# Kernel tuning notes

Hardware: AMD Instinct MI355X
Metric: run time of the kernel (lower is better)

The kernel has to match this reference:

```python
import jax, jax.numpy as jnp
import numpy as np

B, N, C = 1, 512, 128  # batch, seq (pair rows/cols), pair channel dim
EPS = 1e-5
ENDING = False  # 'outgoing' triangle update (ending=False in the torch module)


def layer_norm(x, w, b):
    mu = jnp.mean(x, axis=-1, keepdims=True)
    var = jnp.mean(jnp.square(x - mu), axis=-1, keepdims=True)
    return (x - mu) * jax.lax.rsqrt(var + EPS) * w + b


def setup_inputs() -> dict:
    key = jax.random.key(0)
    ks = jax.random.split(key, 10)
    s = 0.02
    return {
        "x": jax.random.normal(ks[0], (B, N, N, C), dtype=jnp.float32),
        "norm_in_w": jnp.ones((C,), jnp.float32),
        "norm_in_b": jnp.zeros((C,), jnp.float32),
        "g_in_w": jax.random.normal(ks[1], (2 * C, C), jnp.float32) * s,
        "p_in_w": jax.random.normal(ks[2], (2 * C, C), jnp.float32) * s,
        "g_out_w": jax.random.normal(ks[3], (C, C), jnp.float32) * s,
        "norm_out_w": jnp.ones((C,), jnp.float32),
        "norm_out_b": jnp.zeros((C,), jnp.float32),
        "p_out_w": jax.random.normal(ks[4], (C, C), jnp.float32) * s,
    }


def reference(x, norm_in_w, norm_in_b, g_in_w, p_in_w, g_out_w,
              norm_out_w, norm_out_b, p_out_w):
    # LN -> fused g/p/g_out projections (no bias, as in Boltz)
    xn = layer_norm(x, norm_in_w, norm_in_b)                      # [B,N,N,C]
    g_in = jax.nn.sigmoid(jnp.einsum('bijc,dc->bijd', xn, g_in_w))  # [B,N,N,2C]
    p_in = jnp.einsum('bijc,dc->bijd', xn, p_in_w)                  # [B,N,N,2C]
    pg = p_in * g_in                                                # gated projections
    a = pg[..., :C]   # left projection  [B,N,N,C]
    b = pg[..., C:]   # right projection [B,N,N,C]
    if ENDING:
        tri = jnp.einsum('bkic,bkjc->bijc', a, b)  # incoming edges
    else:
        tri = jnp.einsum('bikc,bjkc->bijc', a, b)  # outgoing edges
    out = layer_norm(tri, norm_out_w, norm_out_b)
    out = jnp.einsum('bijc,dc->bijd', out, p_out_w)                 # [B,N,N,C]
    gate = jax.nn.sigmoid(jnp.einsum('bijc,dc->bijd', xn, g_out_w))
    return out * gate
```

## Files before the change

kernel.cpp:

```cpp
#include <hip/hip_runtime.h>

typedef __bf16 bf16;
typedef __bf16 bf16x4 __attribute__((ext_vector_type(4)));
typedef __bf16 bf16x8 __attribute__((ext_vector_type(8)));
typedef float floatx4 __attribute__((ext_vector_type(4)));

#define NN 512
#define CC 128
#define NROW (NN*NN)

__device__ __forceinline__ void async16(void* lds, const void* g) {
    __builtin_amdgcn_global_load_lds((const __attribute__((address_space(1))) void*)g,
                                     (__attribute__((address_space(3))) void*)lds, 16, 0, 0);
}
__device__ __forceinline__ void wait_vm0() {
    asm volatile("s_waitcnt vmcnt(0)" ::: "memory");
}
__device__ __forceinline__ float sigmoidf(float x) {
    return __builtin_amdgcn_rcpf(1.f + __expf(-x));
}

__global__ void setup_kernel(const float* __restrict__ nin_w, const float* __restrict__ nin_b,
                             const float* __restrict__ g_in_w, const float* __restrict__ p_in_w,
                             const float* __restrict__ g_out_w,
                             const float* __restrict__ nout_w, const float* __restrict__ nout_b,
                             const float* __restrict__ p_out_w,
                             bf16* __restrict__ Wall, float* __restrict__ T1, float* __restrict__ T2,
                             bf16* __restrict__ Pp, float* __restrict__ S1, float* __restrict__ S2) {
    int r = blockIdx.x * 256 + threadIdx.x;
    if (r < 640) {
        const float* src = (r < 256) ? (g_in_w + r*CC)
                         : (r < 512) ? (p_in_w + (r-256)*CC)
                                     : (g_out_w + (r-512)*CC);
        float t1 = 0.f, t2 = 0.f;
        for (int c = 0; c < CC; ++c) {
            float wv = src[c];
            float wn = nin_w[c];
            float bn = nin_b[c];
            Wall[r*CC + c] = (bf16)(wv * wn);
            t1 += wn * wv;
            t2 += bn * wv;
        }
        T1[r] = t1; T2[r] = t2;
    } else if (r < 768) {
        int d = r - 640;
        const float* src = p_out_w + d*CC;
        float t1 = 0.f, t2 = 0.f;
        for (int c = 0; c < CC; ++c) {
            float wv = src[c];
            float wn = nout_w[c];
            float bn = nout_b[c];
            Pp[d*CC + c] = (bf16)(wv * wn);
            t1 += wn * wv;
            t2 += bn * wv;
        }
        S1[d] = t1; S2[d] = t2;
    }
}

__global__ __launch_bounds__(256) void k1_ln_proj(
        const float* __restrict__ x, const bf16* __restrict__ Wall,
        const float* __restrict__ T1, const float* __restrict__ T2,
        bf16* __restrict__ a_t, bf16* __restrict__ b_t, bf16* __restrict__ gate) {
    __shared__ char  XNb[16384];
    __shared__ char  TB[12288];
    __shared__ float MU[64], RS[64];

    const int t    = threadIdx.x;
    const int w    = t >> 6, lane = t & 63;
    const int col  = lane & 15, quad = lane >> 4;
    const long r0  = (long)blockIdx.x * 64;

    const int row  = t >> 2;
    const int part = t & 3;
    const float* xr = x + (r0 + row) * CC;
    floatx4 f[8];
#pragma unroll
    for (int j = 0; j < 8; ++j)
        f[j] = *(const floatx4*)(xr + (j*4 + part)*4);

    {
        float sum = 0.f, ss = 0.f;
#pragma unroll
        for (int j = 0; j < 8; ++j)
#pragma unroll
            for (int e = 0; e < 4; ++e) { float v = f[j][e]; sum += v; ss += v*v; }
        sum += __shfl_xor(sum, 1, 64); ss += __shfl_xor(ss, 1, 64);
        sum += __shfl_xor(sum, 2, 64); ss += __shfl_xor(ss, 2, 64);
        float mu  = sum * (1.f/128.f);
        float var = ss  * (1.f/128.f) - mu*mu;
        float rs  = rsqrtf(var + 1e-5f);
        if (part == 0) { MU[row] = mu; RS[row] = rs; }
    }

#pragma unroll
    for (int j = 0; j < 8; ++j) {
        int c4   = j*4 + part;
        int c16  = c4 >> 1, half = c4 & 1;
        bf16x4 v;
        v[0] = (bf16)f[j][0]; v[1] = (bf16)f[j][1];
        v[2] = (bf16)f[j][2]; v[3] = (bf16)f[j][3];
        *(bf16x4*)(XNb + row*256 + ((c16 ^ (row & 15)) * 16) + half*8) = v;
    }
    __syncthreads();

    char* TBw = TB + w*3072;

    for (int jj = 0; jj < 6; ++jj) {
        int job = w + jj*4;
        if (job < 16) {
            bf16x8 bg[4], bp[4];
            for (int s = 0; s < 4; ++s) {
                bg[s] = *(const bf16x8*)(Wall + (      job*16 + col)*CC + s*32 + quad*8);
                bp[s] = *(const bf16x8*)(Wall + (256 + job*16 + col)*CC + s*32 + quad*8);
            }
            int dg = job*16 + col, dp = 256 + job*16 + col;
            float t1g = T1[dg], t2g = T2[dg], t1p = T1[dp], t2p = T2[dp];
            bf16* dst = (job < 8) ? a_t : b_t;
            int cbase = (job < 8 ? job : job - 8) * 16;
            for (int mt = 0; mt < 4; ++mt) {
                int rr = mt*16 + col;
                bf16x8 afm[4];
            #pragma unroll
                for (int s = 0; s < 4; ++s)
                    afm[s] = *(const bf16x8*)(XNb + rr*256 + (((s*4 + quad) ^ (rr & 15)) * 16));
                floatx4 ag = {0.f,0.f,0.f,0.f}, ap = {0.f,0.f,0.f,0.f};
            #pragma unroll
                for (int s = 0; s < 4; ++s) {
                    ag = __builtin_amdgcn_mfma_f32_16x16x32_bf16(afm[s], bg[s], ag, 0, 0, 0);
                    ap = __builtin_amdgcn_mfma_f32_16x16x32_bf16(afm[s], bp[s], ap, 0, 0, 0);
                }
                bf16x4 pk;
            #pragma unroll
                for (int reg = 0; reg < 4; ++reg) {
                    int m = mt*16 + quad*4 + reg;
                    float rs = RS[m], mu = MU[m];
                    float g = rs*ag[reg] - rs*mu*t1g + t2g;
                    float p = rs*ap[reg] - rs*mu*t1p + t2p;
                    pk[reg] = (bf16)(p * sigmoidf(g));
                }
                *(bf16x4*)(TBw + col*144 + mt*32 + quad*8) = pk;
            }
            {
                int c  = lane >> 2;
                int c0 = lane & 3, c1 = (lane & 3) + 4;
                bf16x8 r0v = *(const bf16x8*)(TBw + c*144 + c0*16);
                bf16x8 r1v = *(const bf16x8*)(TBw + c*144 + c1*16);
                bf16* base = dst + (long)(cbase + c) * NROW + r0;
                *(bf16x8*)(base + c0*8) = r0v;
                *(bf16x8*)(base + c1*8) = r1v;
            }
        } else {
            int gc = job - 16;
            bf16x8 bgt[4];
            for (int s = 0; s < 4; ++s)
                bgt[s] = *(const bf16x8*)(Wall + (512 + gc*16 + col)*CC + s*32 + quad*8);
            int dd = 512 + gc*16 + col;
            float t1 = T1[dd], t2 = T2[dd];
            for (int mt = 0; mt < 4; ++mt) {
                int rr = mt*16 + col;
                bf16x8 afm[4];
            #pragma unroll
                for (int s = 0; s < 4; ++s)
                    afm[s] = *(const bf16x8*)(XNb + rr*256 + (((s*4 + quad) ^ (rr & 15)) * 16));
                floatx4 ac = {0.f,0.f,0.f,0.f};
            #pragma unroll
                for (int s = 0; s < 4; ++s)
                    ac = __builtin_amdgcn_mfma_f32_16x16x32_bf16(afm[s], bgt[s], ac, 0, 0, 0);
            #pragma unroll
                for (int reg = 0; reg < 4; ++reg) {
                    int m = mt*16 + quad*4 + reg;
                    float rs = RS[m], mu = MU[m];
                    float g = rs*ac[reg] - rs*mu*t1 + t2;
                    *(bf16*)(TBw + m*48 + col*2) = (bf16)sigmoidf(g);
                }
            }
            {
                bf16x8 g0 = *(const bf16x8*)(TBw + lane*48 + 0);
                bf16x8 g1 = *(const bf16x8*)(TBw + lane*48 + 16);
                bf16* gdst = gate + (r0 + lane)*CC + gc*16;
                *(bf16x8*)(gdst + 0) = g0;
                *(bf16x8*)(gdst + 8) = g1;
            }
        }
    }
}

__device__ __forceinline__ void k2_stage(char* Asb, char* Bsb, const char* Ac, const char* Bc,
                                         int i0, int j0, int k0, int t) {
    for (int q = 0; q < 4; ++q) {
        int L = q*4096 + t*16;
        int row = L >> 6, p = (L >> 4) & 3;
        int cl = p ^ ((row >> 2) & 3);
        async16(Asb + L, Ac + (i0 + row)*1024 + k0*2 + cl*16);
    }
    for (int q = 0; q < 2; ++q) {
        int L = q*4096 + t*16;
        int row = L >> 6, p = (L >> 4) & 3;
        int cl = p ^ ((row >> 2) & 3);
        async16(Bsb + L, Bc + (j0 + row)*1024 + k0*2 + cl*16);
    }
}

__global__ __launch_bounds__(256, 2) void k2_tri(
        const bf16* __restrict__ a_t, const bf16* __restrict__ b_t, bf16* __restrict__ tri) {
    __shared__ char As[2][16384], Bs[2][8192];
    const int t    = threadIdx.x;
    const int w    = t >> 6, lane = t & 63;
    const int col  = lane & 15, quad = lane >> 4;
    const int wg   = blockIdx.x;
    const int c    = (wg & 7) + ((wg >> 6) << 3);
    const int tile = (wg >> 3) & 7;
    const int i0   = (tile >> 2) * 256, j0 = (tile & 3) * 128;
    const char* Ac = (const char*)(a_t + (long)c * NROW);
    const char* Bc = (const char*)(b_t + (long)c * NROW);
    const int wm = w * 64;

    floatx4 acc[4][8];
    for (int mt = 0; mt < 4; ++mt)
        for (int nt = 0; nt < 8; ++nt) { floatx4 z = {0.f,0.f,0.f,0.f}; acc[mt][nt] = z; }

    k2_stage(As[0], Bs[0], Ac, Bc, i0, j0, 0, t);
    wait_vm0();
    __syncthreads();

    int cur = 0;
    for (int kt = 0; kt < 16; ++kt) {
        if (kt < 15)
            k2_stage(As[cur^1], Bs[cur^1], Ac, Bc, i0, j0, (kt+1)*32, t);
        bf16x8 afr[4], bfr[8];
        for (int mt = 0; mt < 4; ++mt) {
            int row = wm + mt*16 + col;
            afr[mt] = *(const bf16x8*)(As[cur] + row*64 + ((quad ^ ((row>>2)&3))*16));
        }
        for (int nt = 0; nt < 8; ++nt) {
            int row = nt*16 + col;
            bfr[nt] = *(const bf16x8*)(Bs[cur] + row*64 + ((quad ^ ((row>>2)&3))*16));
        }
        for (int mt = 0; mt < 4; ++mt)
            for (int nt = 0; nt < 8; ++nt)
                acc[mt][nt] = __builtin_amdgcn_mfma_f32_16x16x32_bf16(afr[mt], bfr[nt], acc[mt][nt], 0, 0, 0);
        wait_vm0();
        __syncthreads();
        cur ^= 1;
    }
    bf16* Tc = tri + (long)c * NROW;
    for (int mt = 0; mt < 4; ++mt)
        for (int nt = 0; nt < 8; ++nt)
            for (int reg = 0; reg < 4; ++reg) {
                int m = i0 + wm + mt*16 + quad*4 + reg;
                int n = j0 + nt*16 + col;
                Tc[m*512 + n] = (bf16)acc[mt][nt][reg];
            }
}

__global__ __launch_bounds__(256) void k3_out(
        const bf16* __restrict__ tri, const bf16* __restrict__ Pp,
        const float* __restrict__ S1, const float* __restrict__ S2,
        const bf16* __restrict__ gate, float* __restrict__ out) {
    __shared__ char  AS[128*272];
    __shared__ float MU[128], RS[128];
    const int t    = threadIdx.x;
    const int w    = t >> 6, lane = t & 63;
    const int col  = lane & 15, quad = lane >> 4;
    const long r0  = (long)blockIdx.x * 128;

    for (int it = 0; it < 2; ++it) {
        int grp = it*16 + (t >> 4);
        int c0  = grp*4;
        int jb  = (t & 15)*8;
        const bf16* src = tri + (long)c0 * NROW + r0 + jb;
        bf16x8 p0 = *(const bf16x8*)(src);
        bf16x8 p1 = *(const bf16x8*)(src + NROW);
        bf16x8 p2 = *(const bf16x8*)(src + 2*NROW);
        bf16x8 p3 = *(const bf16x8*)(src + 3*NROW);
        int slot = grp ^ ((t & 3) << 1);
    #pragma unroll
        for (int j = 0; j < 8; ++j) {
            bf16x4 v;
            v[0] = p0[j]; v[1] = p1[j]; v[2] = p2[j]; v[3] = p3[j];
            *(bf16x4*)(AS + (jb + j)*272 + slot*8) = v;
        }
    }
    __syncthreads();

    {
        int row = t >> 1, half = t & 1;
        float sum = 0.f, ss = 0.f;
        for (int j = 0; j < 8; ++j) {
            int ch = (half*8 + j) ^ ((row >> 3) & 3);
            bf16x8 v = *(const bf16x8*)(AS + row*272 + ch*16);
            for (int jj = 0; jj < 8; ++jj) { float f = (float)v[jj]; sum += f; ss += f*f; }
        }
        sum += __shfl_xor(sum, 1, 64);
        ss  += __shfl_xor(ss, 1, 64);
        float mu  = sum * (1.f/128.f);
        float var = ss  * (1.f/128.f) - mu*mu;
        float rs  = rsqrtf(var + 1e-5f);
        if (half == 0) { MU[row] = mu; RS[row] = rs; }
    }
    __syncthreads();

    const int wm = (w >> 1)*64, wn = (w & 1)*64;
    floatx4 acc[4][4];
    for (int mt = 0; mt < 4; ++mt)
        for (int nt = 0; nt < 4; ++nt) { floatx4 z = {0.f,0.f,0.f,0.f}; acc[mt][nt] = z; }

    for (int s = 0; s < 4; ++s) {
        bf16x8 bfr[4];
        for (int nt = 0; nt < 4; ++nt)
            bfr[nt] = *(const bf16x8*)(Pp + (wn + nt*16 + col)*CC + s*32 + quad*8);
        for (int mt = 0; mt < 4; ++mt) {
            int row = wm + mt*16 + col;
            int ch  = (s*4 + quad) ^ ((row >> 3) & 3);
            bf16x8 afr = *(const bf16x8*)(AS + row*272 + ch*16);
            for (int nt = 0; nt < 4; ++nt)
                acc[mt][nt] = __builtin_amdgcn_mfma_f32_16x16x32_bf16(afr, bfr[nt], acc[mt][nt], 0, 0, 0);
        }
    }

    for (int mt = 0; mt < 4; ++mt)
        for (int nt = 0; nt < 4; ++nt) {
            int n = wn + nt*16 + col;
            float s1 = S1[n], s2 = S2[n];
            for (int reg = 0; reg < 4; ++reg) {
                int m = wm + mt*16 + quad*4 + reg;
                float rs = RS[m], mu = MU[m];
                float v  = rs*acc[mt][nt][reg] - rs*mu*s1 + s2;
                float gt = (float)gate[(r0 + m)*CC + n];
                out[(r0 + m)*CC + n] = v * gt;
            }
        }
}

extern "C" void kernel_launch(void* const* d_in, const int* in_sizes, int n_in,
                              void* d_out, int out_size, void* d_ws, size_t ws_size,
                              hipStream_t stream) {
    const float* x       = (const float*)d_in[0];
    const float* nin_w   = (const float*)d_in[1];
    const float* nin_b   = (const float*)d_in[2];
    const float* g_in_w  = (const float*)d_in[3];
    const float* p_in_w  = (const float*)d_in[4];
    const float* g_out_w = (const float*)d_in[5];
    const float* nout_w  = (const float*)d_in[6];
    const float* nout_b  = (const float*)d_in[7];
    const float* p_out_w = (const float*)d_in[8];

    char* ws = (char*)d_ws;
    bf16*  Wall = (bf16*)(ws);
    float* T1   = (float*)(ws + 163840);
    float* T2   = (float*)(ws + 166400);
    bf16*  Pp   = (bf16*)(ws + 168960);
    float* S1   = (float*)(ws + 201728);
    float* S2   = (float*)(ws + 202240);
    const long BIG = 67108864L;
    bf16* a_t  = (bf16*)(ws + 204800);
    bf16* b_t  = (bf16*)(ws + 204800 + BIG);
    bf16* gate = (bf16*)(ws + 204800 + 2*BIG);
    bf16* tri  = (bf16*)(ws + 204800 + 3*BIG);
    float* outp = (float*)d_out;

    setup_kernel<<<3, 256, 0, stream>>>(nin_w, nin_b, g_in_w, p_in_w, g_out_w,
                                        nout_w, nout_b, p_out_w,
                                        Wall, T1, T2, Pp, S1, S2);
    k1_ln_proj<<<4096, 256, 0, stream>>>(x, Wall, T1, T2, a_t, b_t, gate);
    k2_tri<<<1024, 256, 0, stream>>>(a_t, b_t, tri);
    k3_out<<<2048, 256, 0, stream>>>(tri, Pp, S1, S2, gate, outp);
}
```

Measured before the change: 515.4 us.

## Triple-buffer k2 async LDS pipeline with partial vmcnt waits; prefetch k1 weights

```diff
diff --git a/kernel.cpp b/kernel.cpp
--- a/kernel.cpp
+++ b/kernel.cpp
@@ -12,9 +12,6 @@
 __device__ __forceinline__ void async16(void* lds, const void* g) {
     __builtin_amdgcn_global_load_lds((const __attribute__((address_space(1))) void*)g,
                                      (__attribute__((address_space(3))) void*)lds, 16, 0, 0);
-}
-__device__ __forceinline__ void wait_vm0() {
-    asm volatile("s_waitcnt vmcnt(0)" ::: "memory");
 }
 __device__ __forceinline__ float sigmoidf(float x) {
     return __builtin_amdgcn_rcpf(1.f + __expf(-x));
@@ -106,18 +103,36 @@
 
     char* TBw = TB + w*3072;
 
+    bf16x8 Bb[2][8];
+#pragma unroll
+    for (int s = 0; s < 4; ++s) {
+        Bb[0][s]   = *(const bf16x8*)(Wall + (      (w)*16 + col)*CC + s*32 + quad*8);
+        Bb[0][4+s] = *(const bf16x8*)(Wall + (256 + (w)*16 + col)*CC + s*32 + quad*8);
+    }
+
+#pragma unroll
     for (int jj = 0; jj < 6; ++jj) {
-        int job = w + jj*4;
-        if (job < 16) {
-            bf16x8 bg[4], bp[4];
+        const int cb = jj & 1, nb = cb ^ 1;
+        const int job = w + jj*4;
+        if (jj < 3) {
+            const int nj = w + (jj+1)*4;
+        #pragma unroll
             for (int s = 0; s < 4; ++s) {
-                bg[s] = *(const bf16x8*)(Wall + (      job*16 + col)*CC + s*32 + quad*8);
-                bp[s] = *(const bf16x8*)(Wall + (256 + job*16 + col)*CC + s*32 + quad*8);
-            }
+                Bb[nb][s]   = *(const bf16x8*)(Wall + (      nj*16 + col)*CC + s*32 + quad*8);
+                Bb[nb][4+s] = *(const bf16x8*)(Wall + (256 + nj*16 + col)*CC + s*32 + quad*8);
+            }
+        } else if (jj < 5) {
+            const int ng = w + (jj+1)*4 - 16;
+        #pragma unroll
+            for (int s = 0; s < 4; ++s)
+                Bb[nb][s] = *(const bf16x8*)(Wall + (512 + ng*16 + col)*CC + s*32 + quad*8);
+        }
+        if (jj < 4) {
             int dg = job*16 + col, dp = 256 + job*16 + col;
             float t1g = T1[dg], t2g = T2[dg], t1p = T1[dp], t2p = T2[dp];
-            bf16* dst = (job < 8) ? a_t : b_t;
-            int cbase = (job < 8 ? job : job - 8) * 16;
+            bf16* dst = (jj < 2) ? a_t : b_t;
+            int cbase = (jj < 2 ? job : job - 8) * 16;
+        #pragma unroll
             for (int mt = 0; mt < 4; ++mt) {
                 int rr = mt*16 + col;
                 bf16x8 afm[4];
@@ -127,8 +142,8 @@
                 floatx4 ag = {0.f,0.f,0.f,0.f}, ap = {0.f,0.f,0.f,0.f};
             #pragma unroll
                 for (int s = 0; s < 4; ++s) {
-                    ag = __builtin_amdgcn_mfma_f32_16x16x32_bf16(afm[s], bg[s], ag, 0, 0, 0);
-                    ap = __builtin_amdgcn_mfma_f32_16x16x32_bf16(afm[s], bp[s], ap, 0, 0, 0);
+                    ag = __builtin_amdgcn_mfma_f32_16x16x32_bf16(afm[s], Bb[cb][s],   ag, 0, 0, 0);
+                    ap = __builtin_amdgcn_mfma_f32_16x16x32_bf16(afm[s], Bb[cb][4+s], ap, 0, 0, 0);
                 }
                 bf16x4 pk;
             #pragma unroll
@@ -151,12 +166,10 @@
                 *(bf16x8*)(base + c1*8) = r1v;
             }
         } else {
-            int gc = job - 16;
-            bf16x8 bgt[4];
-            for (int s = 0; s < 4; ++s)
-                bgt[s] = *(const bf16x8*)(Wall + (512 + gc*16 + col)*CC + s*32 + quad*8);
+            const int gc = job - 16;
             int dd = 512 + gc*16 + col;
             float t1 = T1[dd], t2 = T2[dd];
+        #pragma unroll
             for (int mt = 0; mt < 4; ++mt) {
                 int rr = mt*16 + col;
                 bf16x8 afm[4];
@@ -166,7 +179,7 @@
                 floatx4 ac = {0.f,0.f,0.f,0.f};
             #pragma unroll
                 for (int s = 0; s < 4; ++s)
-                    ac = __builtin_amdgcn_mfma_f32_16x16x32_bf16(afm[s], bgt[s], ac, 0, 0, 0);
+                    ac = __builtin_amdgcn_mfma_f32_16x16x32_bf16(afm[s], Bb[cb][s], ac, 0, 0, 0);
             #pragma unroll
                 for (int reg = 0; reg < 4; ++reg) {
                     int m = mt*16 + quad*4 + reg;
@@ -204,7 +217,7 @@
 
 __global__ __launch_bounds__(256, 2) void k2_tri(
         const bf16* __restrict__ a_t, const bf16* __restrict__ b_t, bf16* __restrict__ tri) {
-    __shared__ char As[2][16384], Bs[2][8192];
+    __shared__ char As[3][16384], Bs[3][8192];
     const int t    = threadIdx.x;
     const int w    = t >> 6, lane = t & 63;
     const int col  = lane & 15, quad = lane >> 4;
@@ -220,29 +233,31 @@
     for (int mt = 0; mt < 4; ++mt)
         for (int nt = 0; nt < 8; ++nt) { floatx4 z = {0.f,0.f,0.f,0.f}; acc[mt][nt] = z; }
 
-    k2_stage(As[0], Bs[0], Ac, Bc, i0, j0, 0, t);
-    wait_vm0();
-    __syncthreads();
-
-    int cur = 0;
+    k2_stage(As[0], Bs[0], Ac, Bc, i0, j0, 0,  t);
+    k2_stage(As[1], Bs[1], Ac, Bc, i0, j0, 32, t);
+
     for (int kt = 0; kt < 16; ++kt) {
-        if (kt < 15)
-            k2_stage(As[cur^1], Bs[cur^1], Ac, Bc, i0, j0, (kt+1)*32, t);
+        if (kt < 15) asm volatile("s_waitcnt vmcnt(6)" ::: "memory");
+        else         asm volatile("s_waitcnt vmcnt(0)" ::: "memory");
+        __builtin_amdgcn_s_barrier();
+        if (kt < 14) {
+            int nb = (kt + 2) % 3;
+            k2_stage(As[nb], Bs[nb], Ac, Bc, i0, j0, (kt+2)*32, t);
+        }
+        const char* Ab = As[kt % 3];
+        const char* Bbuf = Bs[kt % 3];
         bf16x8 afr[4], bfr[8];
         for (int mt = 0; mt < 4; ++mt) {
-            int row = wm + mt*16 + col;
-            afr[mt] = *(const bf16x8*)(As[cur] + row*64 + ((quad ^ ((row>>2)&3))*16));
+            int rowm = wm + mt*16 + col;
+            afr[mt] = *(const bf16x8*)(Ab + rowm*64 + ((quad ^ ((rowm>>2)&3))*16));
         }
         for (int nt = 0; nt < 8; ++nt) {
-            int row = nt*16 + col;
-            bfr[nt] = *(const bf16x8*)(Bs[cur] + row*64 + ((quad ^ ((row>>2)&3))*16));
+            int rowm = nt*16 + col;
+            bfr[nt] = *(const bf16x8*)(Bbuf + rowm*64 + ((quad ^ ((rowm>>2)&3))*16));
         }
         for (int mt = 0; mt < 4; ++mt)
             for (int nt = 0; nt < 8; ++nt)
                 acc[mt][nt] = __builtin_amdgcn_mfma_f32_16x16x32_bf16(afr[mt], bfr[nt], acc[mt][nt], 0, 0, 0);
-        wait_vm0();
-        __syncthreads();
-        cur ^= 1;
     }
     bf16* Tc = tri + (long)c * NROW;
     for (int mt = 0; mt < 4; ++mt)
@@ -311,9 +326,9 @@
         for (int nt = 0; nt < 4; ++nt)
             bfr[nt] = *(const bf16x8*)(Pp + (wn + nt*16 + col)*CC + s*32 + quad*8);
         for (int mt = 0; mt < 4; ++mt) {
-            int row = wm + mt*16 + col;
-            int ch  = (s*4 + quad) ^ ((row >> 3) & 3);
-            bf16x8 afr = *(const bf16x8*)(AS + row*272 + ch*16);
+            int rowm = wm + mt*16 + col;
+            int ch  = (s*4 + quad) ^ ((rowm >> 3) & 3);
+            bf16x8 afr = *(const bf16x8*)(AS + rowm*272 + ch*16);
             for (int nt = 0; nt < 4; ++nt)
                 acc[mt][nt] = __builtin_amdgcn_mfma_f32_16x16x32_bf16(afr, bfr[nt], acc[mt][nt], 0, 0, 0);
         }
```

Result: no change. 516.6 us (+0.2%).
